# Kernel tuning notes

Hardware: AMD Instinct MI355X
Metric: run time of the kernel (lower is better)

The kernel has to match this reference:

```python
import jax, jax.numpy as jnp
import numpy as np

B, N, C, H = 8, 4096, 1024, 16
D = C // H
SCALE = D ** -0.5

def setup_inputs() -> dict:
    key = jax.random.key(0)
    ks = jax.random.split(key, 6)
    s = C ** -0.5
    return {
        "fea": jax.random.normal(ks[0], (B, N, C), jnp.float32),
        "embedding": jax.random.normal(ks[1], (B, 1, C), jnp.float32),
        "Wq": jax.random.normal(ks[2], (C, C), jnp.float32) * s,
        "Wk": jax.random.normal(ks[3], (C, C), jnp.float32) * s,
        "Wv": jax.random.normal(ks[4], (C, C), jnp.float32) * s,
        "Wp": jax.random.normal(ks[5], (C, C), jnp.float32) * s,
        "bp": jnp.zeros((C,), jnp.float32),
    }

def reference(fea, embedding, Wq, Wk, Wv, Wp, bp):
    # q: [B,N,H,D]; k,v: [B,H,D] (kv seq len is 1)
    q = (fea @ Wq.T).reshape(B, N, H, D)
    k = (embedding @ Wk.T).reshape(B, H, D)
    v = (embedding @ Wv.T).reshape(B, H, D)
    # attn scores [B,N,H]: single-token key -> per-head dot product
    attn = jax.nn.sigmoid(jnp.einsum("bnhd,bhd->bnh", q, k) * SCALE)
    # broadcast-weight v over sequence: [B,N,H,D] -> [B,N,C]
    feat = (attn[..., None] * v[:, None, :, :]).reshape(B, N, C)
    feat = feat @ Wp.T + bp
    return feat + fea
```

## Files before the change

kernel.cpp:

```cpp
#include <hip/hip_runtime.h>
#include <hip/hip_bf16.h>
#include <stdint.h>

#define B 8
#define N 4096
#define C 1024
#define H 16
#define D 64

static __device__ __forceinline__ float bf_lo(uint32_t u) {
    union { uint32_t i; float f; } c; c.i = u << 16; return c.f;
}
static __device__ __forceinline__ float bf_hi(uint32_t u) {
    union { uint32_t i; float f; } c; c.i = u & 0xffff0000u; return c.f;
}

__global__ __launch_bounds__(256, 2)
void kv_kernel(const float* __restrict__ emb,
               const float* __restrict__ Wk,
               const float* __restrict__ Wv,
               float* __restrict__ kbuf,
               float* __restrict__ vbuf) {
    int wave = (blockIdx.x * blockDim.x + threadIdx.x) >> 6;
    int lane = threadIdx.x & 63;
    int r = wave;
    const float* Wrow = (r < C) ? (Wk + (size_t)r * C) : (Wv + (size_t)(r - C) * C);
    float4 w4[4];
#pragma unroll
    for (int j = 0; j < 4; ++j) w4[j] = *(const float4*)(Wrow + (lane + 64 * j) * 4);
    float acc[B];
#pragma unroll
    for (int b = 0; b < B; ++b) {
        const float* e = emb + (size_t)b * C;
        float a = 0.f;
#pragma unroll
        for (int j = 0; j < 4; ++j) {
            float4 e4 = *(const float4*)(e + (lane + 64 * j) * 4);
            a += w4[j].x * e4.x + w4[j].y * e4.y + w4[j].z * e4.z + w4[j].w * e4.w;
        }
        acc[b] = a;
    }
#pragma unroll
    for (int off = 32; off; off >>= 1)
#pragma unroll
        for (int b = 0; b < B; ++b) acc[b] += __shfl_xor(acc[b], off, 64);
    if (lane == 0) {
        float* dst = (r < C) ? (kbuf + r) : (vbuf + (r - C));
#pragma unroll
        for (int b = 0; b < B; ++b) dst[b * C] = acc[b];
    }
}

__global__ __launch_bounds__(256)
void wu_kernel(const float* __restrict__ Wq,
               const float* __restrict__ Wp,
               const float* __restrict__ kbuf,
               const float* __restrict__ vbuf,
               __hip_bfloat16* __restrict__ wbuf,
               __hip_bfloat16* __restrict__ ubuf) {
    int id = blockIdx.x;
    int t = threadIdx.x;
    if (id < 64) {
        int h = id >> 2;
        int c = ((id & 3) << 8) + t;
        const float* kk = kbuf + h * D;
        float acc[B];
#pragma unroll
        for (int b = 0; b < B; ++b) acc[b] = 0.f;
#pragma unroll 4
        for (int d = 0; d < D; ++d) {
            float wv = Wq[(size_t)(h * D + d) * C + c];
#pragma unroll
            for (int b = 0; b < B; ++b) acc[b] += kk[(size_t)b * C + d] * wv;
        }
#pragma unroll
        for (int b = 0; b < B; ++b)
            wbuf[(size_t)(b * H + h) * C + c] = __float2bfloat16(acc[b]);
    } else {
        int id2 = id - 64;
        int h = id2 >> 2;
        int cp = ((id2 & 3) << 8) + t;
        const float* vv = vbuf + h * D;
        float aq[4][B];
#pragma unroll
        for (int q = 0; q < 4; ++q)
#pragma unroll
            for (int b = 0; b < B; ++b) aq[q][b] = 0.f;
#pragma unroll
        for (int q = 0; q < 4; ++q) {
#pragma unroll
            for (int m = 0; m < 4; ++m) {
                int d0 = q * 16 + m * 4;
                float4 w4 = *(const float4*)(Wp + (size_t)cp * C + h * D + d0);
#pragma unroll
                for (int b = 0; b < B; ++b) {
                    const float* vb = vv + (size_t)b * C + d0;
                    aq[q][b] += w4.x * vb[0] + w4.y * vb[1]
                              + w4.z * vb[2] + w4.w * vb[3];
                }
            }
        }
#pragma unroll
        for (int b = 0; b < B; ++b)
            ubuf[(size_t)(b * H + h) * C + cp] =
                __float2bfloat16((aq[0][b] + aq[1][b]) + (aq[2][b] + aq[3][b]));
    }
}

__global__ __launch_bounds__(512, 4)
void main_kernel(const float* __restrict__ fea,
                 const __hip_bfloat16* __restrict__ wbuf,
                 const __hip_bfloat16* __restrict__ ubuf,
                 const float* __restrict__ bp,
                 float* __restrict__ out) {
    __shared__ uint32_t w_s[H * C / 2];
    __shared__ uint32_t u_s[H * C / 2];
    const int b = blockIdx.y;
    const int tile = blockIdx.x;
    const int tid = threadIdx.x;

    {
        const uint4* wsrc = (const uint4*)(wbuf + (size_t)b * H * C);
        const uint4* usrc = (const uint4*)(ubuf + (size_t)b * H * C);
        uint4* wdst = (uint4*)w_s;
        uint4* udst = (uint4*)u_s;
#pragma unroll
        for (int i = 0; i < H * C / 8 / 512; ++i) {
            wdst[tid + i * 512] = wsrc[tid + i * 512];
            udst[tid + i * 512] = usrc[tid + i * 512];
        }
    }
    __syncthreads();

    const int lane = tid & 63;
    const int wv = tid >> 6;
    const int row0 = tile * 64 + wv * 8;

    float4 bp4[4];
#pragma unroll
    for (int j = 0; j < 4; ++j) bp4[j] = *(const float4*)(bp + 4 * lane + 256 * j);

    const float* fbase = fea + ((size_t)b * N + row0) * C + 4 * lane;
    float* obase = out + ((size_t)b * N + row0) * C + 4 * lane;

#pragma unroll 1
    for (int g = 0; g < 4; ++g) {
        float4 f[2][4];
#pragma unroll
        for (int r = 0; r < 2; ++r)
#pragma unroll
            for (int j = 0; j < 4; ++j)
                f[r][j] = *(const float4*)(fbase + (size_t)(2 * g + r) * C + 256 * j);

        float4 acc[2][4];
#pragma unroll
        for (int r = 0; r < 2; ++r)
#pragma unroll
            for (int j = 0; j < 4; ++j) {
                acc[r][j].x = f[r][j].x + bp4[j].x;
                acc[r][j].y = f[r][j].y + bp4[j].y;
                acc[r][j].z = f[r][j].z + bp4[j].z;
                acc[r][j].w = f[r][j].w + bp4[j].w;
            }

#pragma unroll 1
        for (int h = 0; h < H; ++h) {
            const uint32_t* wrow = w_s + h * (C / 2) + 2 * lane;
            float s[2];
            s[0] = 0.f; s[1] = 0.f;
#pragma unroll
            for (int j = 0; j < 4; ++j) {
                uint2 p = *(const uint2*)(wrow + 128 * j);
                float lx = bf_lo(p.x), hx = bf_hi(p.x);
                float ly = bf_lo(p.y), hy = bf_hi(p.y);
#pragma unroll
                for (int r = 0; r < 2; ++r)
                    s[r] += f[r][j].x * lx + f[r][j].y * hx
                          + f[r][j].z * ly + f[r][j].w * hy;
            }
#pragma unroll
            for (int off = 32; off; off >>= 1)
#pragma unroll
                for (int r = 0; r < 2; ++r) s[r] += __shfl_xor(s[r], off, 64);
#pragma unroll
            for (int r = 0; r < 2; ++r)
                s[r] = 1.f / (1.f + __expf(-0.125f * s[r]));

            const uint32_t* urow = u_s + h * (C / 2) + 2 * lane;
#pragma unroll
            for (int j = 0; j < 4; ++j) {
                uint2 p = *(const uint2*)(urow + 128 * j);
                float lx = bf_lo(p.x), hx = bf_hi(p.x);
                float ly = bf_lo(p.y), hy = bf_hi(p.y);
#pragma unroll
                for (int r = 0; r < 2; ++r) {
                    acc[r][j].x += s[r] * lx; acc[r][j].y += s[r] * hx;
                    acc[r][j].z += s[r] * ly; acc[r][j].w += s[r] * hy;
                }
            }
        }

#pragma unroll
        for (int r = 0; r < 2; ++r)
#pragma unroll
            for (int j = 0; j < 4; ++j)
                *(float4*)(obase + (size_t)(2 * g + r) * C + 256 * j) = acc[r][j];
    }
}

extern "C" void kernel_launch(void* const* d_in, const int* in_sizes, int n_in,
                              void* d_out, int out_size, void* d_ws, size_t ws_size,
                              hipStream_t stream) {
    const float* fea = (const float*)d_in[0];
    const float* emb = (const float*)d_in[1];
    const float* Wq  = (const float*)d_in[2];
    const float* Wk  = (const float*)d_in[3];
    const float* Wv  = (const float*)d_in[4];
    const float* Wp  = (const float*)d_in[5];
    const float* bp  = (const float*)d_in[6];
    float* out = (float*)d_out;

    char* ws = (char*)d_ws;
    float* kbuf = (float*)ws;
    float* vbuf = (float*)(ws + 32 * 1024);
    __hip_bfloat16* wbuf = (__hip_bfloat16*)(ws + 64 * 1024);
    __hip_bfloat16* ubuf = (__hip_bfloat16*)(ws + 320 * 1024);

    hipLaunchKernelGGL(kv_kernel, dim3(2 * C / 4), dim3(256), 0, stream,
                       emb, Wk, Wv, kbuf, vbuf);
    hipLaunchKernelGGL(wu_kernel, dim3(128), dim3(256), 0, stream,
                       Wq, Wp, kbuf, vbuf, wbuf, ubuf);
    hipLaunchKernelGGL(main_kernel, dim3(N / 64, B), dim3(512), 0, stream,
                       fea, wbuf, ubuf, bp, out);
}
```

Measured before the change: 286.1 us.

## Double waves per block, use DPP reductions and split score/accumulate phases

Main kernel now runs 1024-thread blocks with each wave handling 4 rows, doubling resident waves per CU under the fixed shared-memory footprint. The cross-lane sum uses DPP row-shift/broadcast ops instead of shuffle butterflies, with results published by lane 63 through a small LDS buffer. The attention scale is folded into the precomputed W buffer, and the bias add is deferred so the separate accumulator registers disappear. Risks include relying on intra-wave LDS ordering without a barrier and higher per-block register limits.

```diff
diff --git a/kernel.cpp b/kernel.cpp
--- a/kernel.cpp
+++ b/kernel.cpp
@@ -13,6 +13,20 @@
 }
 static __device__ __forceinline__ float bf_hi(uint32_t u) {
     union { uint32_t i; float f; } c; c.i = u & 0xffff0000u; return c.f;
+}
+
+#define DPP_ADD(s, ctrl, rmask)                                              \
+    s += __int_as_float(__builtin_amdgcn_update_dpp(                         \
+        0, __float_as_int(s), ctrl, rmask, 0xf, true))
+
+static __device__ __forceinline__ float wave_sum_dpp(float s) {
+    DPP_ADD(s, 0x111, 0xf);
+    DPP_ADD(s, 0x112, 0xf);
+    DPP_ADD(s, 0x114, 0xf);
+    DPP_ADD(s, 0x118, 0xf);
+    DPP_ADD(s, 0x142, 0xa);
+    DPP_ADD(s, 0x143, 0xc);
+    return s;
 }
 
 __global__ __launch_bounds__(256, 2)
@@ -75,7 +89,7 @@
         }
 #pragma unroll
         for (int b = 0; b < B; ++b)
-            wbuf[(size_t)(b * H + h) * C + c] = __float2bfloat16(acc[b]);
+            wbuf[(size_t)(b * H + h) * C + c] = __float2bfloat16(0.125f * acc[b]);
     } else {
         int id2 = id - 64;
         int h = id2 >> 2;
@@ -107,7 +121,7 @@
     }
 }
 
-__global__ __launch_bounds__(512, 4)
+__global__ __launch_bounds__(1024, 8)
 void main_kernel(const float* __restrict__ fea,
                  const __hip_bfloat16* __restrict__ wbuf,
                  const __hip_bfloat16* __restrict__ ubuf,
@@ -115,6 +129,7 @@
                  float* __restrict__ out) {
     __shared__ uint32_t w_s[H * C / 2];
     __shared__ uint32_t u_s[H * C / 2];
+    __shared__ float sig_s[16 * H * 2];
     const int b = blockIdx.y;
     const int tile = blockIdx.x;
     const int tid = threadIdx.x;
@@ -125,49 +140,34 @@
         uint4* wdst = (uint4*)w_s;
         uint4* udst = (uint4*)u_s;
 #pragma unroll
-        for (int i = 0; i < H * C / 8 / 512; ++i) {
-            wdst[tid + i * 512] = wsrc[tid + i * 512];
-            udst[tid + i * 512] = usrc[tid + i * 512];
+        for (int i = 0; i < H * C / 8 / 1024; ++i) {
+            wdst[tid + i * 1024] = wsrc[tid + i * 1024];
+            udst[tid + i * 1024] = usrc[tid + i * 1024];
         }
     }
     __syncthreads();
 
     const int lane = tid & 63;
     const int wv = tid >> 6;
-    const int row0 = tile * 64 + wv * 8;
-
-    float4 bp4[4];
-#pragma unroll
-    for (int j = 0; j < 4; ++j) bp4[j] = *(const float4*)(bp + 4 * lane + 256 * j);
+    const int row0 = tile * 64 + wv * 4;
+    float* sigp = sig_s + wv * (H * 2);
 
     const float* fbase = fea + ((size_t)b * N + row0) * C + 4 * lane;
     float* obase = out + ((size_t)b * N + row0) * C + 4 * lane;
 
 #pragma unroll 1
-    for (int g = 0; g < 4; ++g) {
+    for (int g = 0; g < 2; ++g) {
         float4 f[2][4];
 #pragma unroll
         for (int r = 0; r < 2; ++r)
 #pragma unroll
             for (int j = 0; j < 4; ++j)
                 f[r][j] = *(const float4*)(fbase + (size_t)(2 * g + r) * C + 256 * j);
-
-        float4 acc[2][4];
-#pragma unroll
-        for (int r = 0; r < 2; ++r)
-#pragma unroll
-            for (int j = 0; j < 4; ++j) {
-                acc[r][j].x = f[r][j].x + bp4[j].x;
-                acc[r][j].y = f[r][j].y + bp4[j].y;
-                acc[r][j].z = f[r][j].z + bp4[j].z;
-                acc[r][j].w = f[r][j].w + bp4[j].w;
-            }
 
 #pragma unroll 1
         for (int h = 0; h < H; ++h) {
             const uint32_t* wrow = w_s + h * (C / 2) + 2 * lane;
-            float s[2];
-            s[0] = 0.f; s[1] = 0.f;
+            float sp[2][4];
 #pragma unroll
             for (int j = 0; j < 4; ++j) {
                 uint2 p = *(const uint2*)(wrow + 128 * j);
@@ -175,28 +175,44 @@
                 float ly = bf_lo(p.y), hy = bf_hi(p.y);
 #pragma unroll
                 for (int r = 0; r < 2; ++r)
-                    s[r] += f[r][j].x * lx + f[r][j].y * hx
-                          + f[r][j].z * ly + f[r][j].w * hy;
-            }
-#pragma unroll
-            for (int off = 32; off; off >>= 1)
-#pragma unroll
-                for (int r = 0; r < 2; ++r) s[r] += __shfl_xor(s[r], off, 64);
-#pragma unroll
-            for (int r = 0; r < 2; ++r)
-                s[r] = 1.f / (1.f + __expf(-0.125f * s[r]));
-
+                    sp[r][j] = f[r][j].x * lx + f[r][j].y * hx
+                             + f[r][j].z * ly + f[r][j].w * hy;
+            }
+            float s0 = (sp[0][0] + sp[0][1]) + (sp[0][2] + sp[0][3]);
+            float s1 = (sp[1][0] + sp[1][1]) + (sp[1][2] + sp[1][3]);
+            s0 = wave_sum_dpp(s0);
+            s1 = wave_sum_dpp(s1);
+            s0 = 1.f / (1.f + __expf(-s0));
+            s1 = 1.f / (1.f + __expf(-s1));
+            if (lane == 63) *(float2*)(sigp + h * 2) = make_float2(s0, s1);
+        }
+
+        {
+            const float* bpp = bp + 4 * lane;
+#pragma unroll
+            for (int j = 0; j < 4; ++j) {
+                float4 bp4 = *(const float4*)(bpp + 256 * j);
+#pragma unroll
+                for (int r = 0; r < 2; ++r) {
+                    f[r][j].x += bp4.x; f[r][j].y += bp4.y;
+                    f[r][j].z += bp4.z; f[r][j].w += bp4.w;
+                }
+            }
+        }
+
+#pragma unroll 1
+        for (int h = 0; h < H; ++h) {
+            float2 sg = *(const float2*)(sigp + h * 2);
             const uint32_t* urow = u_s + h * (C / 2) + 2 * lane;
 #pragma unroll
             for (int j = 0; j < 4; ++j) {
                 uint2 p = *(const uint2*)(urow + 128 * j);
                 float lx = bf_lo(p.x), hx = bf_hi(p.x);
                 float ly = bf_lo(p.y), hy = bf_hi(p.y);
-#pragma unroll
-                for (int r = 0; r < 2; ++r) {
-                    acc[r][j].x += s[r] * lx; acc[r][j].y += s[r] * hx;
-                    acc[r][j].z += s[r] * ly; acc[r][j].w += s[r] * hy;
-                }
+                f[0][j].x += sg.x * lx; f[0][j].y += sg.x * hx;
+                f[0][j].z += sg.x * ly; f[0][j].w += sg.x * hy;
+                f[1][j].x += sg.y * lx; f[1][j].y += sg.y * hx;
+                f[1][j].z += sg.y * ly; f[1][j].w += sg.y * hy;
             }
         }
 
@@ -204,7 +220,7 @@
         for (int r = 0; r < 2; ++r)
 #pragma unroll
             for (int j = 0; j < 4; ++j)
-                *(float4*)(obase + (size_t)(2 * g + r) * C + 256 * j) = acc[r][j];
+                *(float4*)(obase + (size_t)(2 * g + r) * C + 256 * j) = f[r][j];
     }
 }
 
@@ -230,6 +246,6 @@
                        emb, Wk, Wv, kbuf, vbuf);
     hipLaunchKernelGGL(wu_kernel, dim3(128), dim3(256), 0, stream,
                        Wq, Wp, kbuf, vbuf, wbuf, ubuf);
-    hipLaunchKernelGGL(main_kernel, dim3(N / 64, B), dim3(512), 0, stream,
+    hipLaunchKernelGGL(main_kernel, dim3(N / 64, B), dim3(1024), 0, stream,
                        fea, wbuf, ubuf, bp, out);
 }
```

Result: no change. 282.5 us (-1.3%).
